# Kernel tuning notes

Hardware: AMD Instinct MI355X
Metric: run time of the kernel (lower is better)

Reference implementation:

```python
import jax, jax.numpy as jnp
import numpy as np

ALPHA = 1.0   # alpha=1 -> loss = alpha*loss_shape; temporal term weighted by (1-alpha)=0
GAMMA = 0.01  # soft-DTW smoothing
G = 0.05      # logistic weight steepness (weighted-DTW, Jeong et al. 2011)
BIG = 1e9     # finite 'infinity' (keeps vjp NaN-free vs. true inf)


def _softdtw(D, gamma):
    # Soft-DTW value of cost matrix D [N,N] via anti-diagonal (wavefront) scan.
    # R(i,j) = D[i,j] + softmin_gamma(R(i-1,j-1), R(i-1,j), R(i,j-1)),
    # R(-1,-1)=0, other out-of-range = +inf. Diagonal k holds cells (i, k-i).
    N = D.shape[-1]
    i = jnp.arange(N)

    def step(carry, k):
        r2, r1 = carry            # diagonals k-2 and k-1, indexed by row i
        j = k - i
        valid = (j >= 0) & (j < N)
        dk = jnp.where(valid, D[i, jnp.clip(j, 0, N - 1)], 0.0)
        up = jnp.where(i > 0, jnp.roll(r1, 1), BIG)     # R(i-1, j)
        left = r1                                        # R(i, j-1) (BIG where invalid)
        dg = jnp.where(i > 0, jnp.roll(r2, 1), BIG)      # R(i-1, j-1)
        dg = jnp.where((i == 0) & (j == 0), 0.0, dg)     # R(-1,-1) = 0 boundary
        smin = -gamma * jax.nn.logsumexp(jnp.stack([-dg, -up, -left]) / gamma, axis=0)
        rk = jnp.where(valid, dk + smin, BIG)
        return (r1, rk), None

    r0 = jnp.full((N,), BIG, dtype=D.dtype)
    (_, rlast), _ = jax.lax.scan(step, (r0, r0), jnp.arange(2 * N - 1))
    return rlast[N - 1]  # cell (N-1, N-1)


def _weighted_dilate(inp, tgt):
    B, N, _ = inp.shape
    idx = jnp.arange(N, dtype=inp.dtype)
    # modified-logistic weight on |i-j|, midpoint N/2, steepness g
    w = 1.0 / (1.0 + jnp.exp(-G * (jnp.abs(idx[:, None] - idx[None, :]) - N / 2.0)))
    # pairwise squared euclidean cost: D[b,i,j] = sum_d (tgt[b,i,d]-inp[b,j,d])^2
    D = jnp.sum((tgt[:, :, None, :] - inp[:, None, :, :]) ** 2, axis=-1) * w
    sdtw = jax.vmap(lambda d: _softdtw(d, GAMMA))(D)  # [B]
    loss_shape = jnp.mean(sdtw)
    return ALPHA * loss_shape  # (1-alpha)*loss_temporal == 0 at default alpha=1


def setup_inputs() -> dict:
    key = jax.random.key(0)
    k1, k2 = jax.random.split(key)
    B, N, Dm = 32, 1024, 1
    return {
        "input": jax.random.normal(k1, (B, N, Dm), dtype=jnp.float32),
        "target": jax.random.normal(k2, (B, N, Dm), dtype=jnp.float32),
    }


def reference(input, target):
    return _weighted_dilate(input, target)
```

## Files before the change

### kernel.cpp

```cpp
#include <hip/hip_runtime.h>
#include <math.h>

#define NN 1024
#define BATCH 32
#define P 8
#define NW 4
#define THREADS 256
#define DD 32
#define SW 32
#define SPAN 160
#define NT 64
#define RB 4
#define EXB 4
#define WLN 2368
#define GW 0.05f
#define K2 144.2695040888963f
#define INV_K2 0.0069314718055994531f
#define BIGS 1.4426950408889634e11f

#define EXP2F(x) __builtin_amdgcn_exp2f(x)
#define LOG2F(x) __builtin_amdgcn_logf(x)

typedef unsigned long long u64;

__device__ __forceinline__ float dppshr(float oldv, float src) {
    return __int_as_float(__builtin_amdgcn_update_dpp(
        __float_as_int(oldv), __float_as_int(src), 0x138, 0xF, 0xF, false));
}

__device__ __forceinline__ u64 pk(float v, unsigned tag) {
    return ((u64)tag << 32) | (u64)__float_as_uint(v);
}

__device__ __forceinline__ void waitProg(int* fp, int want) {
    while (__hip_atomic_load(fp, __ATOMIC_ACQUIRE, __HIP_MEMORY_SCOPE_WORKGROUP) < want)
        __builtin_amdgcn_s_sleep(1);
}

__global__ __launch_bounds__(256) void ws_init(int* __restrict__ acks,
                                               u64* __restrict__ gx) {
    if (blockIdx.x == 256) acks[threadIdx.x] = 0;
    else gx[(size_t)blockIdx.x * 256 + threadIdx.x] = 0;
}

#define STEPBODY(d, DOMASK) do {                                              \
        xv = dppshr(((d) == 0) ? xf0 : xv, xv);        \
        const float up = dppshr(((d) == 0) ? bndUp : r1, r1);  \
        const float dg = dgp;                                                 \
        const float left = r1;                                                \
        const float diff = ti - xv;                                           \
        const float dk = diff * diff * wreg[(d)];         \
        const float mn = fminf(fminf(dg, up), left);                          \
        const float md = __builtin_amdgcn_fmed3f(dg, up, left);               \
        const float mx = fmaxf(fmaxf(dg, up), left);                          \
        const float ss = 1.0f + EXP2F(mn - md) + EXP2F(mn - mx);              \
        float r = dk + mn - LOG2F(ss);                                        \
        if (DOMASK) r = (jj0 >= -(d)) ? r : BIGS;        \
        r2 = r1; r1 = r; dgp = up;                                            \
    } while (0)

__global__ __launch_bounds__(THREADS) void sdtw_pipe8(
        const float* __restrict__ inp, const float* __restrict__ tgt,
        float* __restrict__ partial, int* __restrict__ acks,
        u64* __restrict__ gx)
{
    __shared__ __align__(16) float xs[NN];
    __shared__ __align__(16) float wlu[WLN];
    __shared__ float2 exch[EXB][SPAN];
    __shared__ int prog[NW];

    const int bid = blockIdx.x;
    const int b = bid & 31;
    const int p = bid >> 5;
    const int tid = threadIdx.x;
    const int w = tid >> 6;
    const int lane = tid & 63;

    const int mlo = 767 - 256 * p;
    for (int tdx = tid; tdx < NN; tdx += THREADS)
        xs[tdx] = inp[b * NN + tdx];
    for (int tdx = tid; tdx < WLN; tdx += THREADS) {
        int m = tdx + mlo;
        float val = K2;
        if ((unsigned)m <= 2046u)
            val = K2 / (1.0f + __expf(-GW * (fabsf((float)m - 1023.0f) - 512.0f)));
        wlu[tdx] = val;
    }
    if (tid < NW) prog[tid] = -1;

    const int i = 128 * p - (DD - 1) + SW * w + lane;
    const int i0 = i - lane;
    const bool rowValid = (unsigned)i < (unsigned)NN;
    int ic = min(max(i, 0), NN - 1);
    const float ti = tgt[b * NN + ic];
    const int imask = rowValid ? i : 0x3FFFFFFF;
    const int wq = 256 + 256 * p - 2 * i;

    float r1 = BIGS, r2 = BIGS;
    float dgp = (i == 0) ? 0.0f : BIGS;
    float bndUp = BIGS;
    float xv = 0.0f;
    int ackC = 0;

    __syncthreads();

    const int fin = b * P + p;
    const int fout = fin + 1;
    u64* gout = gx + (size_t)fout * (RB * DD * 2);
    u64* ginb = gx + (size_t)fin * (RB * DD * 2);

    const bool isProd = (w == NW - 1) && (p < P - 1);
    const bool isCons = (w == 0) && (p > 0);

    u64 pfA = 0, pfB = 0, pfC0 = 0, pfC1 = 0;
    float nr1 = 0.0f, nr2 = 0.0f, nbx = 0.0f, nby = 0.0f;

    int cP  = min(max(-1 - i, 0), NN - 1);
    int c0P = min(max(-i0, 0), NN - 1);
    float xpreA = xs[cP];
    float xpreB = xs[c0P];

    float wreg[DD];
    {
        const float* wp = &wlu[wq];
        #pragma unroll
        for (int h = 0; h < DD / 2; ++h) {
            float2 w2 = *reinterpret_cast<const float2*>(&wp[2 * h]);
            wreg[2 * h] = w2.x; wreg[2 * h + 1] = w2.y;
        }
    }

    for (int t = 0; t < NT; ++t) {
        if (t > 0) {
            if (isProd) {
                if (t > RB) {
                    while (ackC < t - RB) {
                        __builtin_amdgcn_s_sleep(1);
                        ackC = __hip_atomic_load(&acks[fout], __ATOMIC_RELAXED,
                                                 __HIP_MEMORY_SCOPE_AGENT);
                    }
                }
                if (lane >= DD - 1 && lane < 63) {
                    u64* gq = gout + (size_t)((t - 1) & (RB - 1)) * (DD * 2)
                                   + (size_t)(lane - (DD - 1)) * 2;
                    __hip_atomic_store(&gq[0], pk(r1, (unsigned)t),
                                       __ATOMIC_RELAXED, __HIP_MEMORY_SCOPE_AGENT);
                    __hip_atomic_store(&gq[1], pk(r2, (unsigned)t),
                                       __ATOMIC_RELAXED, __HIP_MEMORY_SCOPE_AGENT);
                }
                ackC = __hip_atomic_load(&acks[fout], __ATOMIC_RELAXED,
                                         __HIP_MEMORY_SCOPE_AGENT);
            }
            if (w > 0) {
                if (lane < DD - 1) { r1 = nr1; r2 = nr2; }
                float nd = dppshr(0.0f, r2);
                if (lane == 0)           { bndUp = nbx; dgp = nby; }
                else if (lane <= DD - 2) dgp = nd;
            } else if (p > 0) {
                const unsigned expect = (unsigned)t;
                const u64* gslot = ginb + (size_t)((t - 1) & (RB - 1)) * (DD * 2);
                for (;;) {
                    int ok = 1;
                    if (lane < DD - 1)
                        ok = ((unsigned)(pfA >> 32) == expect) &
                             ((unsigned)(pfB >> 32) == expect);
                    if (lane == 0)
                        ok &= ((unsigned)(pfC0 >> 32) == expect) &
                              ((unsigned)(pfC1 >> 32) == expect);
                    if (__all(ok)) break;
                    if (lane < DD - 1) {
                        pfA = __hip_atomic_load((u64*)&gslot[(size_t)(lane + 1) * 2],
                                                __ATOMIC_RELAXED, __HIP_MEMORY_SCOPE_AGENT);
                        pfB = __hip_atomic_load((u64*)&gslot[(size_t)(lane + 1) * 2 + 1],
                                                __ATOMIC_RELAXED, __HIP_MEMORY_SCOPE_AGENT);
                    }
                    if (lane == 0) {
                        pfC0 = __hip_atomic_load((u64*)&gslot[0],
                                                 __ATOMIC_RELAXED, __HIP_MEMORY_SCOPE_AGENT);
                        pfC1 = __hip_atomic_load((u64*)&gslot[1],
                                                 __ATOMIC_RELAXED, __HIP_MEMORY_SCOPE_AGENT);
                    }
                }
                if (lane < DD - 1) { r1 = __uint_as_float((unsigned)pfA);
                                     r2 = __uint_as_float((unsigned)pfB); }
                float nd = dppshr(0.0f, r2);
                if (lane == 0) { bndUp = __uint_as_float((unsigned)pfC0);
                                 dgp   = __uint_as_float((unsigned)pfC1); }
                else if (lane <= DD - 2) dgp = nd;
                if (lane == 0)
                    __hip_atomic_store(&acks[fin], (int)(pfC0 >> 32),
                                       __ATOMIC_RELAXED, __HIP_MEMORY_SCOPE_AGENT);
            } else {
                bndUp = BIGS;
            }
        }

        const int kbase = t << 5;
        const int jj0 = kbase - imask;

        const float xf0 = xpreB;
        xv = xpreA;
        { int cN  = min(max(kbase + DD - 1 - i, 0), NN - 1);
          int c0N = min(max(kbase + DD - i0, 0), NN - 1);
          xpreA = xs[cN]; xpreB = xs[c0N]; }

        if (i0 >= 0 && kbase >= i0 + 63) {
            #pragma unroll
            for (int d = 0; d < DD; ++d) STEPBODY(d, 0);
        } else {
            #pragma unroll
            for (int d = 0; d < DD; ++d) STEPBODY(d, 1);
        }
        if (t == NT - 1) break;

        if (w < NW - 1) {
            if (t >= EXB - 1) waitProg(&prog[w + 1], t - (EXB - 1));
            if (lane >= DD - 1)
                exch[t & (EXB - 1)][SW * w + lane] = make_float2(r1, r2);
        }
        if (lane == 0)
            __hip_atomic_store(&prog[w], t, __ATOMIC_RELEASE,
                               __HIP_MEMORY_SCOPE_WORKGROUP);

        {
            const float* wp = &wlu[((t + 1) << 5) + wq];
            #pragma unroll
            for (int h = 0; h < DD / 2; ++h) {
                float2 w2 = *reinterpret_cast<const float2*>(&wp[2 * h]);
                wreg[2 * h] = w2.x; wreg[2 * h + 1] = w2.y;
            }
        }

        if (w > 0) {
            waitProg(&prog[w - 1], t);
            const int buf = t & (EXB - 1);
            if (lane < DD - 1) { float2 vv = exch[buf][SW * w + lane]; nr1 = vv.x; nr2 = vv.y; }
            float2 bv = exch[buf][SW * w - 1];
            nbx = bv.x; nby = bv.y;
        }

        if (isCons) {
            const u64* gslot = ginb + (size_t)(t & (RB - 1)) * (DD * 2);
            if (lane < DD - 1) {
                pfA = __hip_atomic_load((u64*)&gslot[(size_t)(lane + 1) * 2],
                                        __ATOMIC_RELAXED, __HIP_MEMORY_SCOPE_AGENT);
                pfB = __hip_atomic_load((u64*)&gslot[(size_t)(lane + 1) * 2 + 1],
                                        __ATOMIC_RELAXED, __HIP_MEMORY_SCOPE_AGENT);
            }
            if (lane == 0) {
                pfC0 = __hip_atomic_load((u64*)&gslot[0],
                                         __ATOMIC_RELAXED, __HIP_MEMORY_SCOPE_AGENT);
                pfC1 = __hip_atomic_load((u64*)&gslot[1],
                                         __ATOMIC_RELAXED, __HIP_MEMORY_SCOPE_AGENT);
            }
        }
    }

    if (i == NN - 1) partial[b] = r2 * INV_K2;
}

__global__ __launch_bounds__(64) void reduce_mean32(const float* __restrict__ partial,
                                                    float* __restrict__ out) {
    float v = (threadIdx.x < BATCH) ? partial[threadIdx.x] : 0.0f;
    #pragma unroll
    for (int off = 32; off > 0; off >>= 1) v += __shfl_down(v, off);
    if (threadIdx.x == 0) out[0] = v * (1.0f / (float)BATCH);
}

extern "C" void kernel_launch(void* const* d_in, const int* in_sizes, int n_in,
                              void* d_out, int out_size, void* d_ws, size_t ws_size,
                              hipStream_t stream) {
    const float* inp = (const float*)d_in[0];
    const float* tgt = (const float*)d_in[1];
    float* out = (float*)d_out;

    float* partial = (float*)d_ws;
    int* acks  = (int*)((char*)d_ws + 128);
    u64* gx    = (u64*)((char*)d_ws + 2048);

    ws_init<<<257, 256, 0, stream>>>(acks, gx);
    sdtw_pipe8<<<BATCH * P, THREADS, 0, stream>>>(inp, tgt, partial, acks, gx);
    reduce_mean32<<<1, 64, 0, stream>>>(partial, out);
}
```

Measured before the change: 206.7 us.

## Move cross-block producer publish and consumer wait to end of step with prefetch

The producer wave now publishes its boundary values for the next step right after computing the current step, not at the start of the next iteration. The consumer wave waits for and loads the incoming boundary at the end of the step, storing it in staging registers the same way the intra-block exchange does, and prefetches the following slot. This shortens the critical path between workgroups in the wavefront pipeline and unifies the w>0 and p>0 input paths. It adds a sleep in the consumer spin loop, and the ring-buffer indexing and ack logic change, which risks ordering errors.

Result: slower. 225.6 us (+9.1%).

```diff
diff --git a/kernel.cpp b/kernel.cpp
--- a/kernel.cpp
+++ b/kernel.cpp
@@ -107,10 +107,11 @@
     const int fin = b * P + p;
     const int fout = fin + 1;
     u64* gout = gx + (size_t)fout * (RB * DD * 2);
-    u64* ginb = gx + (size_t)fin * (RB * DD * 2);
+    const u64* ginb = gx + (size_t)fin * (RB * DD * 2);
 
     const bool isProd = (w == NW - 1) && (p < P - 1);
     const bool isCons = (w == 0) && (p > 0);
+    const bool hasIn = (w > 0) || (p > 0);
 
     u64 pfA = 0, pfB = 0, pfC0 = 0, pfC1 = 0;
     float nr1 = 0.0f, nr2 = 0.0f, nbx = 0.0f, nby = 0.0f;
@@ -130,66 +131,29 @@
         }
     }
 
+    if (isCons) {
+        const u64* gslot = ginb + (size_t)(1 & (RB - 1)) * (DD * 2);
+        if (lane < DD - 1) {
+            pfA = __hip_atomic_load((u64*)&gslot[(size_t)(lane + 1) * 2],
+                                    __ATOMIC_RELAXED, __HIP_MEMORY_SCOPE_AGENT);
+            pfB = __hip_atomic_load((u64*)&gslot[(size_t)(lane + 1) * 2 + 1],
+                                    __ATOMIC_RELAXED, __HIP_MEMORY_SCOPE_AGENT);
+        }
+        if (lane == 0) {
+            pfC0 = __hip_atomic_load((u64*)&gslot[0],
+                                     __ATOMIC_RELAXED, __HIP_MEMORY_SCOPE_AGENT);
+            pfC1 = __hip_atomic_load((u64*)&gslot[1],
+                                     __ATOMIC_RELAXED, __HIP_MEMORY_SCOPE_AGENT);
+        }
+    }
+
     for (int t = 0; t < NT; ++t) {
         if (t > 0) {
-            if (isProd) {
-                if (t > RB) {
-                    while (ackC < t - RB) {
-                        __builtin_amdgcn_s_sleep(1);
-                        ackC = __hip_atomic_load(&acks[fout], __ATOMIC_RELAXED,
-                                                 __HIP_MEMORY_SCOPE_AGENT);
-                    }
-                }
-                if (lane >= DD - 1 && lane < 63) {
-                    u64* gq = gout + (size_t)((t - 1) & (RB - 1)) * (DD * 2)
-                                   + (size_t)(lane - (DD - 1)) * 2;
-                    __hip_atomic_store(&gq[0], pk(r1, (unsigned)t),
-                                       __ATOMIC_RELAXED, __HIP_MEMORY_SCOPE_AGENT);
-                    __hip_atomic_store(&gq[1], pk(r2, (unsigned)t),
-                                       __ATOMIC_RELAXED, __HIP_MEMORY_SCOPE_AGENT);
-                }
-                ackC = __hip_atomic_load(&acks[fout], __ATOMIC_RELAXED,
-                                         __HIP_MEMORY_SCOPE_AGENT);
-            }
-            if (w > 0) {
+            if (hasIn) {
                 if (lane < DD - 1) { r1 = nr1; r2 = nr2; }
                 float nd = dppshr(0.0f, r2);
                 if (lane == 0)           { bndUp = nbx; dgp = nby; }
                 else if (lane <= DD - 2) dgp = nd;
-            } else if (p > 0) {
-                const unsigned expect = (unsigned)t;
-                const u64* gslot = ginb + (size_t)((t - 1) & (RB - 1)) * (DD * 2);
-                for (;;) {
-                    int ok = 1;
-                    if (lane < DD - 1)
-                        ok = ((unsigned)(pfA >> 32) == expect) &
-                             ((unsigned)(pfB >> 32) == expect);
-                    if (lane == 0)
-                        ok &= ((unsigned)(pfC0 >> 32) == expect) &
-                              ((unsigned)(pfC1 >> 32) == expect);
-                    if (__all(ok)) break;
-                    if (lane < DD - 1) {
-                        pfA = __hip_atomic_load((u64*)&gslot[(size_t)(lane + 1) * 2],
-                                                __ATOMIC_RELAXED, __HIP_MEMORY_SCOPE_AGENT);
-                        pfB = __hip_atomic_load((u64*)&gslot[(size_t)(lane + 1) * 2 + 1],
-                                                __ATOMIC_RELAXED, __HIP_MEMORY_SCOPE_AGENT);
-                    }
-                    if (lane == 0) {
-                        pfC0 = __hip_atomic_load((u64*)&gslot[0],
-                                                 __ATOMIC_RELAXED, __HIP_MEMORY_SCOPE_AGENT);
-                        pfC1 = __hip_atomic_load((u64*)&gslot[1],
-                                                 __ATOMIC_RELAXED, __HIP_MEMORY_SCOPE_AGENT);
-                    }
-                }
-                if (lane < DD - 1) { r1 = __uint_as_float((unsigned)pfA);
-                                     r2 = __uint_as_float((unsigned)pfB); }
-                float nd = dppshr(0.0f, r2);
-                if (lane == 0) { bndUp = __uint_as_float((unsigned)pfC0);
-                                 dgp   = __uint_as_float((unsigned)pfC1); }
-                else if (lane <= DD - 2) dgp = nd;
-                if (lane == 0)
-                    __hip_atomic_store(&acks[fin], (int)(pfC0 >> 32),
-                                       __ATOMIC_RELAXED, __HIP_MEMORY_SCOPE_AGENT);
             } else {
                 bndUp = BIGS;
             }
@@ -213,6 +177,26 @@
         }
         if (t == NT - 1) break;
 
+        if (isProd) {
+            if (t >= RB) {
+                while (ackC < t + 1 - RB) {
+                    __builtin_amdgcn_s_sleep(1);
+                    ackC = __hip_atomic_load(&acks[fout], __ATOMIC_RELAXED,
+                                             __HIP_MEMORY_SCOPE_AGENT);
+                }
+            }
+            if (lane >= DD - 1 && lane < 63) {
+                u64* gq = gout + (size_t)((t + 1) & (RB - 1)) * (DD * 2)
+                               + (size_t)(lane - (DD - 1)) * 2;
+                __hip_atomic_store(&gq[0], pk(r1, (unsigned)(t + 1)),
+                                   __ATOMIC_RELAXED, __HIP_MEMORY_SCOPE_AGENT);
+                __hip_atomic_store(&gq[1], pk(r2, (unsigned)(t + 1)),
+                                   __ATOMIC_RELAXED, __HIP_MEMORY_SCOPE_AGENT);
+            }
+            ackC = __hip_atomic_load(&acks[fout], __ATOMIC_RELAXED,
+                                     __HIP_MEMORY_SCOPE_AGENT);
+        }
+
         if (w < NW - 1) {
             if (t >= EXB - 1) waitProg(&prog[w + 1], t - (EXB - 1));
             if (lane >= DD - 1)
@@ -237,20 +221,50 @@
             if (lane < DD - 1) { float2 vv = exch[buf][SW * w + lane]; nr1 = vv.x; nr2 = vv.y; }
             float2 bv = exch[buf][SW * w - 1];
             nbx = bv.x; nby = bv.y;
-        }
-
-        if (isCons) {
-            const u64* gslot = ginb + (size_t)(t & (RB - 1)) * (DD * 2);
+        } else if (p > 0) {
+            const unsigned expect = (unsigned)(t + 1);
+            const u64* gslot = ginb + (size_t)((t + 1) & (RB - 1)) * (DD * 2);
+            for (;;) {
+                int ok = 1;
+                if (lane < DD - 1)
+                    ok = ((unsigned)(pfA >> 32) == expect) &
+                         ((unsigned)(pfB >> 32) == expect);
+                if (lane == 0)
+                    ok &= ((unsigned)(pfC0 >> 32) == expect) &
+                          ((unsigned)(pfC1 >> 32) == expect);
+                if (__all(ok)) break;
+                __builtin_amdgcn_s_sleep(1);
+                if (lane < DD - 1) {
+                    pfA = __hip_atomic_load((u64*)&gslot[(size_t)(lane + 1) * 2],
+                                            __ATOMIC_RELAXED, __HIP_MEMORY_SCOPE_AGENT);
+                    pfB = __hip_atomic_load((u64*)&gslot[(size_t)(lane + 1) * 2 + 1],
+                                            __ATOMIC_RELAXED, __HIP_MEMORY_SCOPE_AGENT);
+                }
+                if (lane == 0) {
+                    pfC0 = __hip_atomic_load((u64*)&gslot[0],
+                                             __ATOMIC_RELAXED, __HIP_MEMORY_SCOPE_AGENT);
+                    pfC1 = __hip_atomic_load((u64*)&gslot[1],
+                                             __ATOMIC_RELAXED, __HIP_MEMORY_SCOPE_AGENT);
+                }
+            }
+            if (lane < DD - 1) { nr1 = __uint_as_float((unsigned)pfA);
+                                 nr2 = __uint_as_float((unsigned)pfB); }
+            nbx = __uint_as_float((unsigned)pfC0);
+            nby = __uint_as_float((unsigned)pfC1);
+            if (lane == 0)
+                __hip_atomic_store(&acks[fin], (int)(pfC0 >> 32),
+                                   __ATOMIC_RELAXED, __HIP_MEMORY_SCOPE_AGENT);
+            const u64* gnxt = ginb + (size_t)((t + 2) & (RB - 1)) * (DD * 2);
             if (lane < DD - 1) {
-                pfA = __hip_atomic_load((u64*)&gslot[(size_t)(lane + 1) * 2],
+                pfA = __hip_atomic_load((u64*)&gnxt[(size_t)(lane + 1) * 2],
                                         __ATOMIC_RELAXED, __HIP_MEMORY_SCOPE_AGENT);
-                pfB = __hip_atomic_load((u64*)&gslot[(size_t)(lane + 1) * 2 + 1],
+                pfB = __hip_atomic_load((u64*)&gnxt[(size_t)(lane + 1) * 2 + 1],
                                         __ATOMIC_RELAXED, __HIP_MEMORY_SCOPE_AGENT);
             }
             if (lane == 0) {
-                pfC0 = __hip_atomic_load((u64*)&gslot[0],
+                pfC0 = __hip_atomic_load((u64*)&gnxt[0],
                                          __ATOMIC_RELAXED, __HIP_MEMORY_SCOPE_AGENT);
-                pfC1 = __hip_atomic_load((u64*)&gslot[1],
+                pfC1 = __hip_atomic_load((u64*)&gnxt[1],
                                          __ATOMIC_RELAXED, __HIP_MEMORY_SCOPE_AGENT);
             }
         }
```
